# Kernel optimization log

Measured on AMD Instinct MI355X. Metric: run time of the kernel, lower is better.

## Reference

```python
import jax, jax.numpy as jnp
import numpy as np
from jax import lax

INPUT, HIDDEN, LAYERS, ACTIONS = 512, 128, 2, 10
B, T = 512, 256


def _lstm_layer(x_seq, Wih, Whh, bih, bhh):
    """x_seq: [B,T,D] -> (outputs [B,T,H], h_T [B,H], c_T [B,H]). PyTorch gate order i,f,g,o."""
    Bsz = x_seq.shape[0]
    H = Whh.shape[1]
    # Precompute input projection for all timesteps (one big GEMM).
    x_proj = jnp.einsum('btd,gd->btg', x_seq, Wih) + bih + bhh  # [B,T,4H]

    def step(carry, xt):
        h, c = carry
        gates = xt + h @ Whh.T  # [B,4H]
        i, f, g, o = jnp.split(gates, 4, axis=-1)
        c = jax.nn.sigmoid(f) * c + jax.nn.sigmoid(i) * jnp.tanh(g)
        h = jax.nn.sigmoid(o) * jnp.tanh(c)
        return (h, c), h

    init = (jnp.zeros((Bsz, H), x_seq.dtype), jnp.zeros((Bsz, H), x_seq.dtype))
    (hT, cT), hs = lax.scan(step, init, jnp.swapaxes(x_proj, 0, 1))  # hs: [T,B,H]
    return jnp.swapaxes(hs, 0, 1), hT, cT


def setup_inputs() -> dict:
    key = jax.random.key(0)
    ks = jax.random.split(key, 16)
    s_in = 1.0 / np.sqrt(HIDDEN)

    def u(k, shape):
        return jax.random.uniform(k, shape, jnp.float32, -s_in, s_in)

    return {
        'x': jax.random.normal(ks[0], (B, T, INPUT), jnp.float32),
        'Wih0': u(ks[1], (4 * HIDDEN, INPUT)),
        'Whh0': u(ks[2], (4 * HIDDEN, HIDDEN)),
        'bih0': u(ks[3], (4 * HIDDEN,)),
        'bhh0': u(ks[4], (4 * HIDDEN,)),
        'Wih1': u(ks[5], (4 * HIDDEN, HIDDEN)),
        'Whh1': u(ks[6], (4 * HIDDEN, HIDDEN)),
        'bih1': u(ks[7], (4 * HIDDEN,)),
        'bhh1': u(ks[8], (4 * HIDDEN,)),
        'fc1_w': u(ks[9], (HIDDEN // 2, HIDDEN)),
        'fc1_b': u(ks[10], (HIDDEN // 2,)),
        'fc2_w': u(ks[11], (ACTIONS, HIDDEN // 2)),
        'fc2_b': u(ks[12], (ACTIONS,)),
    }


def reference(x, Wih0, Whh0, bih0, bhh0, Wih1, Whh1, bih1, bhh1, fc1_w, fc1_b, fc2_w, fc2_b):
    # Layer 0 (input 512 -> hidden 128); dropout is inference-off (identity).
    h0_seq, h0, c0 = _lstm_layer(x, Wih0, Whh0, bih0, bhh0)
    # Layer 1 (hidden 128 -> hidden 128)
    h1_seq, h1, c1 = _lstm_layer(h0_seq, Wih1, Whh1, bih1, bhh1)
    last = h1_seq[:, -1, :]  # [B,H]
    hid = jax.nn.relu(last @ fc1_w.T + fc1_b)
    logits = hid @ fc2_w.T + fc2_b
    probs = jax.nn.softmax(logits, axis=-1)
    h_n = jnp.stack([h0, h1], axis=0)  # [num_layers,B,H]
    c_n = jnp.stack([c0, c1], axis=0)
    return probs, h_n, c_n
```

## Files before the change

kernel.cpp:

```cpp
#include <hip/hip_runtime.h>
#include <hip/hip_bf16.h>


#define BATCH 512
#define SEQT  256
#define INPUTD 512
#define HID   128
#define GATES 512
#define RB    4
#define SUBS  16
#define NCH   (SEQT / SUBS)

typedef __bf16 bf16_t;
typedef bf16_t bf16x4 __attribute__((ext_vector_type(4)));
typedef bf16_t bf16x8 __attribute__((ext_vector_type(8)));
typedef float  f32x4  __attribute__((ext_vector_type(4)));

__device__ __forceinline__ float sigm(float x) {
    return __builtin_amdgcn_rcpf(1.f + __expf(-x));
}
__device__ __forceinline__ float tanhfast(float x) {
    float xc = fminf(fmaxf(x, -15.f), 15.f);
    float e = __expf(2.f * xc);
    return (e - 1.f) * __builtin_amdgcn_rcpf(e + 1.f);
}

__global__ __launch_bounds__(256) void cvt_weights(
    const float* __restrict__ w0, const float* __restrict__ w1,
    const float* __restrict__ w2, const float* __restrict__ w3,
    bf16_t* __restrict__ o0, bf16_t* __restrict__ o1,
    bf16_t* __restrict__ o2, bf16_t* __restrict__ o3,
    unsigned* __restrict__ flags)
{
    int b = blockIdx.x;
    if (b == 448) {
        uint4 z = make_uint4(0u, 0u, 0u, 0u);
        #pragma unroll
        for (int i = 0; i < 4; ++i)
            ((uint4*)flags)[i * 256 + threadIdx.x] = z;
        return;
    }
    const float* src; bf16_t* dst; long base;
    if (b < 256)      { src = w0; dst = o0; base = (long)b * 256; }
    else if (b < 320) { src = w1; dst = o1; base = (long)(b - 256) * 256; }
    else if (b < 384) { src = w2; dst = o2; base = (long)(b - 320) * 256; }
    else              { src = w3; dst = o3; base = (long)(b - 384) * 256; }
    long i = base + threadIdx.x;
    float4 v = ((const float4*)src)[i];
    bf16x4 r;
    r[0] = (bf16_t)v.x; r[1] = (bf16_t)v.y;
    r[2] = (bf16_t)v.z; r[3] = (bf16_t)v.w;
    ((bf16x4*)dst)[i] = r;
}

__global__ __launch_bounds__(256) void gemm_mfma(
    const float* __restrict__ A, const bf16_t* __restrict__ W,
    const float* __restrict__ b1, const float* __restrict__ b2,
    float* __restrict__ out,
    int K, int tcs, int tcmask, int srcT, int t0)
{
    __shared__ bf16_t As[128 * 32];
    __shared__ bf16_t Bs[128 * 32];
    int tid = threadIdx.x;
    int l = tid & 63;
    int w = tid >> 6;
    int wm = w >> 1, wn = w & 1;
    int bn = blockIdx.x;
    int bm = blockIdx.y;
    int Tc = tcmask + 1;

    long aoff[2], boff[2];
    #pragma unroll
    for (int c = 0; c < 2; ++c) {
        int m = bm * 128 + (tid >> 2) + 64 * c;
        int xr = ((m >> tcs) * srcT) + t0 + (m & tcmask);
        aoff[c] = (long)xr * K + (tid & 3) * 8;
        int n = bn * 128 + (tid >> 2) + 64 * c;
        boff[c] = (long)n * K + (tid & 3) * 8;
    }

    f32x4 acc[4][4];
    #pragma unroll
    for (int i = 0; i < 4; ++i)
        #pragma unroll
        for (int j = 0; j < 4; ++j)
            acc[i][j] = (f32x4){0.f, 0.f, 0.f, 0.f};

    const int rbase = wm * 64 + (l & 15);
    const int cbase = wn * 64 + (l & 15);
    const int kfrag = (l >> 4) * 8;

    for (int kt = 0; kt < K; kt += 32) {
        float4 av[2][2];
        #pragma unroll
        for (int c = 0; c < 2; ++c) {
            av[c][0] = *(const float4*)(A + aoff[c] + kt);
            av[c][1] = *(const float4*)(A + aoff[c] + kt + 4);
        }
        __builtin_amdgcn_global_load_lds(
            (const __attribute__((address_space(1))) void*)(W + boff[0] + kt),
            (__attribute__((address_space(3))) void*)(Bs + tid * 8), 16, 0, 0);
        __builtin_amdgcn_global_load_lds(
            (const __attribute__((address_space(1))) void*)(W + boff[1] + kt),
            (__attribute__((address_space(3))) void*)(Bs + 2048 + tid * 8), 16, 0, 0);
        #pragma unroll
        for (int c = 0; c < 2; ++c) {
            bf16x8 ab;
            ab[0] = (bf16_t)av[c][0].x; ab[1] = (bf16_t)av[c][0].y;
            ab[2] = (bf16_t)av[c][0].z; ab[3] = (bf16_t)av[c][0].w;
            ab[4] = (bf16_t)av[c][1].x; ab[5] = (bf16_t)av[c][1].y;
            ab[6] = (bf16_t)av[c][1].z; ab[7] = (bf16_t)av[c][1].w;
            *(bf16x8*)(As + c * 2048 + tid * 8) = ab;
        }
        __syncthreads();

        bf16x8 af[4], bfr[4];
        #pragma unroll
        for (int i = 0; i < 4; ++i)
            af[i] = *(const bf16x8*)(As + (rbase + i * 16) * 32 + kfrag);
        #pragma unroll
        for (int j = 0; j < 4; ++j)
            bfr[j] = *(const bf16x8*)(Bs + (cbase + j * 16) * 32 + kfrag);

        #pragma unroll
        for (int i = 0; i < 4; ++i)
            #pragma unroll
            for (int j = 0; j < 4; ++j)
                acc[i][j] = __builtin_amdgcn_mfma_f32_16x16x32_bf16(
                    af[i], bfr[j], acc[i][j], 0, 0, 0);
        __syncthreads();
    }

    #pragma unroll
    for (int i = 0; i < 4; ++i) {
        int m0 = bm * 128 + wm * 64 + i * 16 + (l >> 4) * 4;
        #pragma unroll
        for (int j = 0; j < 4; ++j) {
            int n = bn * 128 + wn * 64 + j * 16 + (l & 15);
            float bb = b1[n] + b2[n];
            int hid = n & 127;
            #pragma unroll
            for (int r = 0; r < 4; ++r) {
                int m = m0 + r;
                int b = m >> tcs;
                int t = m & tcmask;
                int br = b >> 2, brow = b & 3;
                out[(((long)br * Tc + t) * 4 + bn) * 512 + brow * 128 + hid] =
                    acc[i][j][r] + bb;
            }
        }
    }
}

#define BARRIER_()                                                             \
    do {                                                                       \
        asm volatile("s_waitcnt lgkmcnt(0)" ::: "memory");                     \
        __builtin_amdgcn_s_barrier();                                          \
        __builtin_amdgcn_sched_barrier(0);                                     \
    } while (0)

#define REC0_STEP(X, t)                                                        \
    {                                                                          \
        bf16x8 a[4];                                                           \
        _Pragma("unroll")                                                      \
        for (int ks = 0; ks < 4; ++ks) {                                       \
            int ba = (col * 256 + ks * 64 + lgroup * 16) ^ ((col & 7) << 4);   \
            a[ks] = *(const bf16x8*)((const char*)h_lds + ba);                 \
        }                                                                      \
        f32x4 acc[4];                                                          \
        _Pragma("unroll")                                                      \
        for (int g = 0; g < 4; ++g) acc[g] = (f32x4){0.f, 0.f, 0.f, 0.f};      \
        _Pragma("unroll")                                                      \
        for (int ks = 0; ks < 4; ++ks)                                         \
            _Pragma("unroll")                                                  \
            for (int g = 0; g < 4; ++g)                                        \
                acc[g] = __builtin_amdgcn_mfma_f32_16x16x32_bf16(              \
                    a[ks], __builtin_bit_cast(bf16x8, wreg[g][ks]), acc[g],    \
                    0, 0, 0);                                                  \
        if (lgroup == 0) {                                                     \
            _Pragma("unroll")                                                  \
            for (int r = 0; r < 4; ++r) {                                      \
                f32x4 v;                                                       \
                v[0] = acc[0][r]; v[1] = acc[1][r];                            \
                v[2] = acc[2][r]; v[3] = acc[3][r];                            \
                *(f32x4*)((char*)g_lds + r * 2048 + coff * 16) = v;            \
            }                                                                  \
        }                                                                      \
        BARRIER_();                                                            \
        {                                                                      \
            f32x4 gv = *(const f32x4*)((const char*)g_lds + tid * 16);         \
            float zi = gv[0] + X.x, zf = gv[1] + X.y;                          \
            float zg = gv[2] + X.z, zo = gv[3] + X.w;                          \
            c = sigm(zf) * c + sigm(zi) * tanhfast(zg);                        \
            h = sigm(zo) * tanhfast(c);                                        \
            *(bf16_t*)((char*)h_lds + hba) = (bf16_t)h;                        \
            h0qp[(long)(t) * 512] = (bf16_t)h;                                 \
        }                                                                      \
        if ((t) + 2 < Tc) {                                                    \
            long o = (long)((t) + 2) * 2048;                                   \
            X.x = xpt[o];        X.y = xpt[o + 512];                           \
            X.z = xpt[o + 1024]; X.w = xpt[o + 1536];                          \
        }                                                                      \
        if (((t) & (SUBS - 1)) == SUBS - 1)                                    \
            asm volatile("s_waitcnt vmcnt(0)" ::: "memory");                   \
        BARRIER_();                                                            \
        if ((((t) & (SUBS - 1)) == SUBS - 1) && tid == 0) {                    \
            __threadfence();                                                   \
            __hip_atomic_store(flagp + ((t) >> 4), 1u, __ATOMIC_RELEASE,       \
                               __HIP_MEMORY_SCOPE_AGENT);                      \
        }                                                                      \
    }

__global__ __launch_bounds__(512, 2) void lstm_dual(
    const float* __restrict__ xp4,
    const bf16_t* __restrict__ Wh0,
    const bf16_t* __restrict__ Wi1,
    const bf16_t* __restrict__ Wh1,
    const float* __restrict__ bih1, const float* __restrict__ bhh1,
    bf16_t* __restrict__ h0q,
    unsigned* __restrict__ flags,
    float* __restrict__ h0st, float* __restrict__ c0st,
    float* __restrict__ h1st, float* __restrict__ c1st,
    int Tc, int first, int subbase)
{
    __shared__ __align__(16) char pool[28 * 1024];
    int tid = threadIdx.x;
    int l = tid & 63;
    int wv = tid >> 6;
    int pair = blockIdx.x & 127;
    int r0 = pair * RB;
    int col = l & 15;
    int lgroup = l >> 4;
    int kreg = lgroup * 8;
    int erow = tid >> 7, ehid = tid & 127;
    const int hba = (erow * 256 + ehid * 2) ^ ((erow & 7) << 4);
    unsigned* flagp = flags + pair * NCH + subbase;

    if (blockIdx.x < 128) {
        bf16_t* h_lds = (bf16_t*)pool;
        float*  g_lds = (float*)(pool + 4096);
        int coff = wv * 16 + col;

        f32x4 wreg[4][4];
        #pragma unroll
        for (int g = 0; g < 4; ++g)
            #pragma unroll
            for (int ks = 0; ks < 4; ++ks)
                wreg[g][ks] = *(const f32x4*)(Wh0 + (long)(g * 128 + coff) * HID
                                              + ks * 32 + kreg);
        #pragma unroll
        for (int g = 0; g < 4; ++g)
            #pragma unroll
            for (int ks = 0; ks < 4; ++ks)
                asm volatile("" : "+a"(wreg[g][ks]));

        float c = first ? 0.f : c0st[(r0 + erow) * HID + ehid];
        float h = first ? 0.f : h0st[(r0 + erow) * HID + ehid];

        ((float2*)h_lds)[tid & 255] = make_float2(0.f, 0.f);
        __syncthreads();
        *(bf16_t*)((char*)h_lds + hba) = (bf16_t)h;
        __syncthreads();

        const float* xpt = xp4 + (long)pair * Tc * 2048 + tid;
        bf16_t* h0qp = h0q + (long)pair * Tc * 512 + (hba >> 1);
        float4 xA, xB;
        xA.x = xpt[0];    xA.y = xpt[512];
        xA.z = xpt[1024]; xA.w = xpt[1536];
        if (Tc > 1) {
            xB.x = xpt[2048];        xB.y = xpt[2048 + 512];
            xB.z = xpt[2048 + 1024]; xB.w = xpt[2048 + 1536];
        } else {
            xB = make_float4(0.f, 0.f, 0.f, 0.f);
        }

        for (int tt = 0; tt < Tc; tt += 2) {
            REC0_STEP(xA, tt)
            REC0_STEP(xB, tt + 1)
        }

        h0st[(r0 + erow) * HID + ehid] = h;
        c0st[(r0 + erow) * HID + ehid] = c;
    } else {
        bf16_t* h0stg = (bf16_t*)pool;
        bf16_t* h1_lds = (bf16_t*)(pool + 8192);
        float*  g1a = (float*)(pool + 12288);
        float*  g1b = (float*)(pool + 20480);
        int isWi = wv < 4;
        int w4 = wv & 3;
        int coff1 = w4 * 32;

        const bf16_t* Wsrc = isWi ? Wi1 : Wh1;
        f32x4 wreg[2][4][4];
        #pragma unroll
        for (int c2 = 0; c2 < 2; ++c2)
            #pragma unroll
            for (int g = 0; g < 4; ++g)
                #pragma unroll
                for (int ks = 0; ks < 4; ++ks)
                    wreg[c2][g][ks] = *(const f32x4*)(
                        Wsrc + (long)(g * 128 + coff1 + c2 * 16 + col) * HID
                        + ks * 32 + kreg);
        #pragma unroll
        for (int c2 = 0; c2 < 2; ++c2)
            #pragma unroll
            for (int g = 0; g < 4; ++g)
                #pragma unroll
                for (int ks = 0; ks < 4; ++ks)
                    asm volatile("" : "+a"(wreg[c2][g][ks]));

        float4 bias1;
        bias1.x = bih1[ehid]       + bhh1[ehid];
        bias1.y = bih1[128 + ehid] + bhh1[128 + ehid];
        bias1.z = bih1[256 + ehid] + bhh1[256 + ehid];
        bias1.w = bih1[384 + ehid] + bhh1[384 + ehid];

        float c1 = first ? 0.f : c1st[(r0 + erow) * HID + ehid];
        float h1 = first ? 0.f : h1st[(r0 + erow) * HID + ehid];

        ((float2*)pool)[tid] = make_float2(0.f, 0.f);
        ((float2*)pool)[tid + 512] = make_float2(0.f, 0.f);
        ((float2*)(pool + 8192))[tid & 255] = make_float2(0.f, 0.f);
        __syncthreads();
        *(bf16_t*)((char*)h1_lds + hba) = (bf16_t)h1;
        __syncthreads();

        if (wv == 0) {
            while (__hip_atomic_load(flagp, __ATOMIC_ACQUIRE,
                                     __HIP_MEMORY_SCOPE_AGENT) == 0u)
                __builtin_amdgcn_s_sleep(2);
            __builtin_amdgcn_global_load_lds(
                (const __attribute__((address_space(1))) void*)(
                    h0q + (long)pair * Tc * 512 + l * 8),
                (__attribute__((address_space(3))) void*)h0stg, 16, 0, 0);
            asm volatile("s_waitcnt vmcnt(0)" ::: "memory");
        }
        __syncthreads();

        for (int t = 0; t < Tc; ++t) {
            int pw = (t + 1) & 3;
            if (t + 1 < Tc && wv == pw) {
                if (((t + 1) & (SUBS - 1)) == 0) {
                    unsigned* fp = flagp + ((t + 1) >> 4);
                    while (__hip_atomic_load(fp, __ATOMIC_ACQUIRE,
                                             __HIP_MEMORY_SCOPE_AGENT) == 0u)
                        __builtin_amdgcn_s_sleep(2);
                }
                __builtin_amdgcn_global_load_lds(
                    (const __attribute__((address_space(1))) void*)(
                        h0q + ((long)pair * Tc + t + 1) * 512 + l * 8),
                    (__attribute__((address_space(3))) void*)(
                        h0stg + ((t + 1) & 1) * 2048), 16, 0, 0);
            }

            const char* asrc = isWi
                ? (const char*)(h0stg + (t & 1) * 2048)
                : (const char*)h1_lds;
            bf16x8 a[4];
            #pragma unroll
            for (int ks = 0; ks < 4; ++ks) {
                int ba = (col * 256 + ks * 64 + lgroup * 16) ^ ((col & 7) << 4);
                a[ks] = *(const bf16x8*)(asrc + ba);
            }
            float* gdst = isWi ? g1a : g1b;
            #pragma unroll
            for (int c2 = 0; c2 < 2; ++c2) {
                f32x4 acc[4];
                #pragma unroll
                for (int g = 0; g < 4; ++g) acc[g] = (f32x4){0.f, 0.f, 0.f, 0.f};
                #pragma unroll
                for (int ks = 0; ks < 4; ++ks)
                    #pragma unroll
                    for (int g = 0; g < 4; ++g)
                        acc[g] = __builtin_amdgcn_mfma_f32_16x16x32_bf16(
                            a[ks], __builtin_bit_cast(bf16x8, wreg[c2][g][ks]),
                            acc[g], 0, 0, 0);
                if (lgroup == 0) {
                    #pragma unroll
                    for (int r = 0; r < 4; ++r) {
                        f32x4 v;
                        v[0] = acc[0][r]; v[1] = acc[1][r];
                        v[2] = acc[2][r]; v[3] = acc[3][r];
                        *(f32x4*)((char*)gdst + r * 2048 +
                                  (coff1 + c2 * 16 + col) * 16) = v;
                    }
                }
            }
            BARRIER_();

            {
                f32x4 gva = *(const f32x4*)((const char*)g1a + tid * 16);
                f32x4 gvb = *(const f32x4*)((const char*)g1b + tid * 16);
                float zi = gva[0] + gvb[0] + bias1.x;
                float zf = gva[1] + gvb[1] + bias1.y;
                float zg = gva[2] + gvb[2] + bias1.z;
                float zo = gva[3] + gvb[3] + bias1.w;
                c1 = sigm(zf) * c1 + sigm(zi) * tanhfast(zg);
                h1 = sigm(zo) * tanhfast(c1);
                *(bf16_t*)((char*)h1_lds + hba) = (bf16_t)h1;
            }
            if (t + 1 < Tc && wv == pw)
                asm volatile("s_waitcnt vmcnt(0)" ::: "memory");
            BARRIER_();
        }

        h1st[(r0 + erow) * HID + ehid] = h1;
        c1st[(r0 + erow) * HID + ehid] = c1;
    }
}

__global__ __launch_bounds__(128) void fc_head(
    const float* __restrict__ h0st, const float* __restrict__ c0st,
    const float* __restrict__ h1st, const float* __restrict__ c1st,
    const float* __restrict__ fc1w, const float* __restrict__ fc1b,
    const float* __restrict__ fc2w, const float* __restrict__ fc2b,
    float* __restrict__ out)
{
    __shared__ float h1_s[HID];
    __shared__ float hid_s[64];
    __shared__ float log_s[10];
    int t = threadIdx.x;
    int b = blockIdx.x;

    h1_s[t] = h1st[b * HID + t];
    __syncthreads();

    if (t < 64) {
        float a = fc1b[t];
        const float* wrow = fc1w + t * HID;
        #pragma unroll 4
        for (int k = 0; k < HID; ++k) a = fmaf(wrow[k], h1_s[k], a);
        hid_s[t] = fmaxf(a, 0.f);
    }
    __syncthreads();

    if (t < 10) {
        float a = fc2b[t];
        const float* wrow = fc2w + t * 64;
        #pragma unroll 4
        for (int k = 0; k < 64; ++k) a = fmaf(wrow[k], hid_s[k], a);
        log_s[t] = a;
    }
    __syncthreads();

    if (t == 0) {
        float m = log_s[0];
        #pragma unroll
        for (int j = 1; j < 10; ++j) m = fmaxf(m, log_s[j]);
        float e[10];
        float s = 0.f;
        #pragma unroll
        for (int j = 0; j < 10; ++j) { e[j] = __expf(log_s[j] - m); s += e[j]; }
        float inv = __builtin_amdgcn_rcpf(s);
        #pragma unroll
        for (int j = 0; j < 10; ++j) out[b * 10 + j] = e[j] * inv;
    }

    float* hn = out + BATCH * 10;
    float* cn = hn + 2 * BATCH * HID;
    hn[b * HID + t] = h0st[b * HID + t];
    hn[BATCH * HID + b * HID + t] = h1_s[t];
    cn[b * HID + t] = c0st[b * HID + t];
    cn[BATCH * HID + b * HID + t] = c1st[b * HID + t];
}

extern "C" void kernel_launch(void* const* d_in, const int* in_sizes, int n_in,
                              void* d_out, int out_size, void* d_ws, size_t ws_size,
                              hipStream_t stream) {
    const float* x    = (const float*)d_in[0];
    const float* Wih0 = (const float*)d_in[1];
    const float* Whh0 = (const float*)d_in[2];
    const float* bih0 = (const float*)d_in[3];
    const float* bhh0 = (const float*)d_in[4];
    const float* Wih1 = (const float*)d_in[5];
    const float* Whh1 = (const float*)d_in[6];
    const float* bih1 = (const float*)d_in[7];
    const float* bhh1 = (const float*)d_in[8];
    const float* fc1w = (const float*)d_in[9];
    const float* fc1b = (const float*)d_in[10];
    const float* fc2w = (const float*)d_in[11];
    const float* fc2b = (const float*)d_in[12];
    float* out = (float*)d_out;

    int Tc = SEQT;
    while (Tc > SUBS) {
        size_t need = (size_t)BATCH * Tc * GATES * 4
                    + ((size_t)GATES * INPUTD + 3 * (size_t)GATES * HID) * 2
                    + (size_t)128 * Tc * 512 * 2
                    + 4 * (size_t)BATCH * HID * 4
                    + 128 * NCH * 4 + 512;
        if (need <= ws_size) break;
        Tc >>= 1;
    }
    int tcs = __builtin_ctz((unsigned)Tc);

    float*    xp   = (float*)d_ws;
    bf16_t*   wb0  = (bf16_t*)(xp + (size_t)BATCH * Tc * GATES);
    bf16_t*   wb1  = wb0 + (size_t)GATES * INPUTD;
    bf16_t*   wh0b = wb1 + (size_t)GATES * HID;
    bf16_t*   wh1b = wh0b + (size_t)GATES * HID;
    bf16_t*   h0q  = wh1b + (size_t)GATES * HID;
    float*    h0st = (float*)(h0q + (size_t)128 * Tc * 512);
    float*    c0st = h0st + (size_t)BATCH * HID;
    float*    h1st = c0st + (size_t)BATCH * HID;
    float*    c1st = h1st + (size_t)BATCH * HID;
    unsigned* flags = (unsigned*)(c1st + (size_t)BATCH * HID);

    cvt_weights<<<449, 256, 0, stream>>>(Wih0, Wih1, Whh0, Whh1,
                                         wb0, wb1, wh0b, wh1b, flags);

    int nchunk = SEQT / Tc;
    dim3 gemm_grid(GATES / 128, (BATCH * Tc) / 128);

    for (int ci = 0; ci < nchunk; ++ci) {
        gemm_mfma<<<gemm_grid, 256, 0, stream>>>(
            x, wb0, bih0, bhh0, xp, INPUTD, tcs, Tc - 1, SEQT, ci * Tc);
        lstm_dual<<<256, 512, 0, stream>>>(
            xp, wh0b, wb1, wh1b, bih1, bhh1, h0q, flags,
            h0st, c0st, h1st, c1st, Tc, ci == 0, ci * (Tc / SUBS));
    }

    fc_head<<<BATCH, 128, 0, stream>>>(
        h0st, c0st, h1st, c1st, fc1w, fc1b, fc2w, fc2b, out);
}
```

Measured before the change: 586.7 us.

## Move layer-1 input projection into layer-0 recurrence block, stream fp32 gate preactivations

The layer-0 block now also holds the layer-1 input weights and computes Wi1·h0 alongside its own recurrent MFMA, writing fp32 gate preactivations for layer 1 to global memory. The layer-1 block then runs only its own recurrent MFMA and reads those preactivations behind chunk flags, instead of staging h0 through LDS and splitting waves between two GEMMs. This shortens the layer-1 critical path per step and frees LDS. In exchange, layer 0 does twice the MFMA work per step, needs more accumulator registers, and writes a 4x larger fp32 intermediate buffer, which may also shrink the time-chunk size when workspace is tight.

Result: slower. 850.1 us (+44.9%).

```diff
diff --git a/kernel.cpp b/kernel.cpp
--- a/kernel.cpp
+++ b/kernel.cpp
@@ -160,6 +160,72 @@
     } while (0)
 
 #define REC0_STEP(X, t)                                                        \
+    {                                                                          \
+        bf16x8 a[4];                                                           \
+        _Pragma("unroll")                                                      \
+        for (int ks = 0; ks < 4; ++ks) {                                       \
+            int ba = (col * 256 + ks * 64 + lgroup * 16) ^ ((col & 7) << 4);   \
+            a[ks] = *(const bf16x8*)((const char*)h_lds + ba);                 \
+        }                                                                      \
+        f32x4 acc0[4], acc1[4];                                                \
+        _Pragma("unroll")                                                      \
+        for (int g = 0; g < 4; ++g) {                                          \
+            acc0[g] = (f32x4){0.f, 0.f, 0.f, 0.f};                             \
+            acc1[g] = (f32x4){0.f, 0.f, 0.f, 0.f};                             \
+        }                                                                      \
+        _Pragma("unroll")                                                      \
+        for (int ks = 0; ks < 4; ++ks)                                         \
+            _Pragma("unroll")                                                  \
+            for (int g = 0; g < 4; ++g) {                                      \
+                acc0[g] = __builtin_amdgcn_mfma_f32_16x16x32_bf16(             \
+                    a[ks], __builtin_bit_cast(bf16x8, wreg[g][ks]), acc0[g],   \
+                    0, 0, 0);                                                  \
+                acc1[g] = __builtin_amdgcn_mfma_f32_16x16x32_bf16(             \
+                    a[ks], __builtin_bit_cast(bf16x8, wi[g][ks]), acc1[g],     \
+                    0, 0, 0);                                                  \
+            }                                                                  \
+        if (lgroup == 0) {                                                     \
+            _Pragma("unroll")                                                  \
+            for (int r = 0; r < 4; ++r) {                                      \
+                f32x4 v;                                                       \
+                v[0] = acc0[0][r]; v[1] = acc0[1][r];                          \
+                v[2] = acc0[2][r]; v[3] = acc0[3][r];                          \
+                *(f32x4*)((char*)g_lds + r * 2048 + coff * 16) = v;            \
+            }                                                                  \
+            if ((t) > 0) {                                                     \
+                float* yt = yqbase + (long)((t) - 1) * 2048;                   \
+                _Pragma("unroll")                                              \
+                for (int g = 0; g < 4; ++g)                                    \
+                    _Pragma("unroll")                                          \
+                    for (int r = 0; r < 4; ++r)                                \
+                        yt[g * 512 + r * 128 + coff] = acc1[g][r];             \
+            }                                                                  \
+        }                                                                      \
+        if ((((t) & (SUBS - 1)) == 0) && (t) > 0)                              \
+            asm volatile("s_waitcnt vmcnt(0)" ::: "memory");                   \
+        BARRIER_();                                                            \
+        if ((((t) & (SUBS - 1)) == 0) && (t) > 0 && tid == 0) {                \
+            __threadfence();                                                   \
+            __hip_atomic_store(flagp + ((t) >> 4) - 1, 1u, __ATOMIC_RELEASE,   \
+                               __HIP_MEMORY_SCOPE_AGENT);                      \
+        }                                                                      \
+        {                                                                      \
+            f32x4 gv = *(const f32x4*)((const char*)g_lds + tid * 16);         \
+            float zi = gv[0] + X.x, zf = gv[1] + X.y;                          \
+            float zg = gv[2] + X.z, zo = gv[3] + X.w;                          \
+            c = sigm(zf) * c + sigm(zi) * tanhfast(zg);                        \
+            h = sigm(zo) * tanhfast(c);                                        \
+            *(bf16_t*)((char*)h_lds + hba) = (bf16_t)h;                        \
+        }                                                                      \
+        if ((t) + 2 < Tc) {                                                    \
+            long o = (long)((t) + 2) * 2048;                                   \
+            X.x = xpt[o];        X.y = xpt[o + 512];                           \
+            X.z = xpt[o + 1024]; X.w = xpt[o + 1536];                          \
+        }                                                                      \
+        BARRIER_();                                                            \
+    }
+
+#define REC1_STEP(Y, t)                                                        \
     {                                                                          \
         bf16x8 a[4];                                                           \
         _Pragma("unroll")                                                      \
@@ -189,26 +255,24 @@
         BARRIER_();                                                            \
         {                                                                      \
             f32x4 gv = *(const f32x4*)((const char*)g_lds + tid * 16);         \
-            float zi = gv[0] + X.x, zf = gv[1] + X.y;                          \
-            float zg = gv[2] + X.z, zo = gv[3] + X.w;                          \
+            float zi = gv[0] + Y.x + bias1.x, zf = gv[1] + Y.y + bias1.y;      \
+            float zg = gv[2] + Y.z + bias1.z, zo = gv[3] + Y.w + bias1.w;      \
             c = sigm(zf) * c + sigm(zi) * tanhfast(zg);                        \
             h = sigm(zo) * tanhfast(c);                                        \
             *(bf16_t*)((char*)h_lds + hba) = (bf16_t)h;                        \
-            h0qp[(long)(t) * 512] = (bf16_t)h;                                 \
         }                                                                      \
         if ((t) + 2 < Tc) {                                                    \
+            if ((((t) + 2) & (SUBS - 1)) == 0) {                               \
+                unsigned* fp = flagp + (((t) + 2) >> 4);                       \
+                while (__hip_atomic_load(fp, __ATOMIC_ACQUIRE,                 \
+                                         __HIP_MEMORY_SCOPE_AGENT) == 0u)      \
+                    __builtin_amdgcn_s_sleep(2);                               \
+            }                                                                  \
             long o = (long)((t) + 2) * 2048;                                   \
-            X.x = xpt[o];        X.y = xpt[o + 512];                           \
-            X.z = xpt[o + 1024]; X.w = xpt[o + 1536];                          \
-        }                                                                      \
-        if (((t) & (SUBS - 1)) == SUBS - 1)                                    \
-            asm volatile("s_waitcnt vmcnt(0)" ::: "memory");                   \
+            Y.x = yqt[o];        Y.y = yqt[o + 512];                           \
+            Y.z = yqt[o + 1024]; Y.w = yqt[o + 1536];                          \
+        }                                                                      \
         BARRIER_();                                                            \
-        if ((((t) & (SUBS - 1)) == SUBS - 1) && tid == 0) {                    \
-            __threadfence();                                                   \
-            __hip_atomic_store(flagp + ((t) >> 4), 1u, __ATOMIC_RELEASE,       \
-                               __HIP_MEMORY_SCOPE_AGENT);                      \
-        }                                                                      \
     }
 
 __global__ __launch_bounds__(512, 2) void lstm_dual(
@@ -217,13 +281,13 @@
     const bf16_t* __restrict__ Wi1,
     const bf16_t* __restrict__ Wh1,
     const float* __restrict__ bih1, const float* __restrict__ bhh1,
-    bf16_t* __restrict__ h0q,
+    float* __restrict__ yq,
     unsigned* __restrict__ flags,
     float* __restrict__ h0st, float* __restrict__ c0st,
     float* __restrict__ h1st, float* __restrict__ c1st,
     int Tc, int first, int subbase)
 {
-    __shared__ __align__(16) char pool[28 * 1024];
+    __shared__ __align__(16) char pool[12 * 1024];
     int tid = threadIdx.x;
     int l = tid & 63;
     int wv = tid >> 6;
@@ -232,27 +296,31 @@
     int col = l & 15;
     int lgroup = l >> 4;
     int kreg = lgroup * 8;
+    int coff = wv * 16 + col;
     int erow = tid >> 7, ehid = tid & 127;
     const int hba = (erow * 256 + ehid * 2) ^ ((erow & 7) << 4);
     unsigned* flagp = flags + pair * NCH + subbase;
 
+    bf16_t* h_lds = (bf16_t*)pool;
+    float*  g_lds = (float*)(pool + 4096);
+
     if (blockIdx.x < 128) {
-        bf16_t* h_lds = (bf16_t*)pool;
-        float*  g_lds = (float*)(pool + 4096);
-        int coff = wv * 16 + col;
-
-        f32x4 wreg[4][4];
+        f32x4 wreg[4][4], wi[4][4];
         #pragma unroll
         for (int g = 0; g < 4; ++g)
             #pragma unroll
-            for (int ks = 0; ks < 4; ++ks)
-                wreg[g][ks] = *(const f32x4*)(Wh0 + (long)(g * 128 + coff) * HID
-                                              + ks * 32 + kreg);
+            for (int ks = 0; ks < 4; ++ks) {
+                long o = (long)(g * 128 + coff) * HID + ks * 32 + kreg;
+                wreg[g][ks] = *(const f32x4*)(Wh0 + o);
+                wi[g][ks]   = *(const f32x4*)(Wi1 + o);
+            }
         #pragma unroll
         for (int g = 0; g < 4; ++g)
             #pragma unroll
-            for (int ks = 0; ks < 4; ++ks)
+            for (int ks = 0; ks < 4; ++ks) {
                 asm volatile("" : "+a"(wreg[g][ks]));
+                asm volatile("" : "+a"(wi[g][ks]));
+            }
 
         float c = first ? 0.f : c0st[(r0 + erow) * HID + ehid];
         float h = first ? 0.f : h0st[(r0 + erow) * HID + ehid];
@@ -263,7 +331,7 @@
         __syncthreads();
 
         const float* xpt = xp4 + (long)pair * Tc * 2048 + tid;
-        bf16_t* h0qp = h0q + (long)pair * Tc * 512 + (hba >> 1);
+        float* yqbase = yq + (long)pair * Tc * 2048;
         float4 xA, xB;
         xA.x = xpt[0];    xA.y = xpt[512];
         xA.z = xpt[1024]; xA.w = xpt[1536];
@@ -279,35 +347,55 @@
             REC0_STEP(xB, tt + 1)
         }
 
+        {
+            bf16x8 a[4];
+            #pragma unroll
+            for (int ks = 0; ks < 4; ++ks) {
+                int ba = (col * 256 + ks * 64 + lgroup * 16) ^ ((col & 7) << 4);
+                a[ks] = *(const bf16x8*)((const char*)h_lds + ba);
+            }
+            f32x4 acc1[4];
+            #pragma unroll
+            for (int g = 0; g < 4; ++g) acc1[g] = (f32x4){0.f, 0.f, 0.f, 0.f};
+            #pragma unroll
+            for (int ks = 0; ks < 4; ++ks)
+                #pragma unroll
+                for (int g = 0; g < 4; ++g)
+                    acc1[g] = __builtin_amdgcn_mfma_f32_16x16x32_bf16(
+                        a[ks], __builtin_bit_cast(bf16x8, wi[g][ks]), acc1[g],
+                        0, 0, 0);
+            if (lgroup == 0) {
+                float* yt = yqbase + (long)(Tc - 1) * 2048;
+                #pragma unroll
+                for (int g = 0; g < 4; ++g)
+                    #pragma unroll
+                    for (int r = 0; r < 4; ++r)
+                        yt[g * 512 + r * 128 + coff] = acc1[g][r];
+            }
+            asm volatile("s_waitcnt vmcnt(0)" ::: "memory");
+            BARRIER_();
+            if (tid == 0) {
+                __threadfence();
+                __hip_atomic_store(flagp + NCH - 1, 1u, __ATOMIC_RELEASE,
+                                   __HIP_MEMORY_SCOPE_AGENT);
+            }
+        }
+
         h0st[(r0 + erow) * HID + ehid] = h;
         c0st[(r0 + erow) * HID + ehid] = c;
     } else {
-        bf16_t* h0stg = (bf16_t*)pool;
-        bf16_t* h1_lds = (bf16_t*)(pool + 8192);
-        float*  g1a = (float*)(pool + 12288);
-        float*  g1b = (float*)(pool + 20480);
-        int isWi = wv < 4;
-        int w4 = wv & 3;
-        int coff1 = w4 * 32;
-
-        const bf16_t* Wsrc = isWi ? Wi1 : Wh1;
-        f32x4 wreg[2][4][4];
-        #pragma unroll
-        for (int c2 = 0; c2 < 2; ++c2)
-            #pragma unroll
-            for (int g = 0; g < 4; ++g)
-                #pragma unroll
-                for (int ks = 0; ks < 4; ++ks)
-                    wreg[c2][g][ks] = *(const f32x4*)(
-                        Wsrc + (long)(g * 128 + coff1 + c2 * 16 + col) * HID
-                        + ks * 32 + kreg);
-        #pragma unroll
-        for (int c2 = 0; c2 < 2; ++c2)
-            #pragma unroll
-            for (int g = 0; g < 4; ++g)
-                #pragma unroll
-                for (int ks = 0; ks < 4; ++ks)
-                    asm volatile("" : "+a"(wreg[c2][g][ks]));
+        f32x4 wreg[4][4];
+        #pragma unroll
+        for (int g = 0; g < 4; ++g)
+            #pragma unroll
+            for (int ks = 0; ks < 4; ++ks)
+                wreg[g][ks] = *(const f32x4*)(
+                    Wh1 + (long)(g * 128 + coff) * HID + ks * 32 + kreg);
+        #pragma unroll
+        for (int g = 0; g < 4; ++g)
+            #pragma unroll
+            for (int ks = 0; ks < 4; ++ks)
+                asm volatile("" : "+a"(wreg[g][ks]));
 
         float4 bias1;
         bias1.x = bih1[ehid]       + bhh1[ehid];
@@ -315,97 +403,35 @@
         bias1.z = bih1[256 + ehid] + bhh1[256 + ehid];
         bias1.w = bih1[384 + ehid] + bhh1[384 + ehid];
 
-        float c1 = first ? 0.f : c1st[(r0 + erow) * HID + ehid];
-        float h1 = first ? 0.f : h1st[(r0 + erow) * HID + ehid];
-
-        ((float2*)pool)[tid] = make_float2(0.f, 0.f);
-        ((float2*)pool)[tid + 512] = make_float2(0.f, 0.f);
-        ((float2*)(pool + 8192))[tid & 255] = make_float2(0.f, 0.f);
+        float c = first ? 0.f : c1st[(r0 + erow) * HID + ehid];
+        float h = first ? 0.f : h1st[(r0 + erow) * HID + ehid];
+
+        ((float2*)h_lds)[tid & 255] = make_float2(0.f, 0.f);
         __syncthreads();
-        *(bf16_t*)((char*)h1_lds + hba) = (bf16_t)h1;
+        *(bf16_t*)((char*)h_lds + hba) = (bf16_t)h;
         __syncthreads();
 
-        if (wv == 0) {
-            while (__hip_atomic_load(flagp, __ATOMIC_ACQUIRE,
-                                     __HIP_MEMORY_SCOPE_AGENT) == 0u)
-                __builtin_amdgcn_s_sleep(2);
-            __builtin_amdgcn_global_load_lds(
-                (const __attribute__((address_space(1))) void*)(
-                    h0q + (long)pair * Tc * 512 + l * 8),
-                (__attribute__((address_space(3))) void*)h0stg, 16, 0, 0);
-            asm volatile("s_waitcnt vmcnt(0)" ::: "memory");
-        }
-        __syncthreads();
-
-        for (int t = 0; t < Tc; ++t) {
-            int pw = (t + 1) & 3;
-            if (t + 1 < Tc && wv == pw) {
-                if (((t + 1) & (SUBS - 1)) == 0) {
-                    unsigned* fp = flagp + ((t + 1) >> 4);
-                    while (__hip_atomic_load(fp, __ATOMIC_ACQUIRE,
-                                             __HIP_MEMORY_SCOPE_AGENT) == 0u)
-                        __builtin_amdgcn_s_sleep(2);
-                }
-                __builtin_amdgcn_global_load_lds(
-                    (const __attribute__((address_space(1))) void*)(
-                        h0q + ((long)pair * Tc + t + 1) * 512 + l * 8),
-                    (__attribute__((address_space(3))) void*)(
-                        h0stg + ((t + 1) & 1) * 2048), 16, 0, 0);
-            }
-
-            const char* asrc = isWi
-                ? (const char*)(h0stg + (t & 1) * 2048)
-                : (const char*)h1_lds;
-            bf16x8 a[4];
-            #pragma unroll
-            for (int ks = 0; ks < 4; ++ks) {
-                int ba = (col * 256 + ks * 64 + lgroup * 16) ^ ((col & 7) << 4);
-                a[ks] = *(const bf16x8*)(asrc + ba);
-            }
-            float* gdst = isWi ? g1a : g1b;
-            #pragma unroll
-            for (int c2 = 0; c2 < 2; ++c2) {
-                f32x4 acc[4];
-                #pragma unroll
-                for (int g = 0; g < 4; ++g) acc[g] = (f32x4){0.f, 0.f, 0.f, 0.f};
-                #pragma unroll
-                for (int ks = 0; ks < 4; ++ks)
-                    #pragma unroll
-                    for (int g = 0; g < 4; ++g)
-                        acc[g] = __builtin_amdgcn_mfma_f32_16x16x32_bf16(
-                            a[ks], __builtin_bit_cast(bf16x8, wreg[c2][g][ks]),
-                            acc[g], 0, 0, 0);
-                if (lgroup == 0) {
-                    #pragma unroll
-                    for (int r = 0; r < 4; ++r) {
-                        f32x4 v;
-                        v[0] = acc[0][r]; v[1] = acc[1][r];
-                        v[2] = acc[2][r]; v[3] = acc[3][r];
-                        *(f32x4*)((char*)gdst + r * 2048 +
-                                  (coff1 + c2 * 16 + col) * 16) = v;
-                    }
-                }
-            }
-            BARRIER_();
-
-            {
-                f32x4 gva = *(const f32x4*)((const char*)g1a + tid * 16);
-                f32x4 gvb = *(const f32x4*)((const char*)g1b + tid * 16);
-                float zi = gva[0] + gvb[0] + bias1.x;
-                float zf = gva[1] + gvb[1] + bias1.y;
-                float zg = gva[2] + gvb[2] + bias1.z;
-                float zo = gva[3] + gvb[3] + bias1.w;
-                c1 = sigm(zf) * c1 + sigm(zi) * tanhfast(zg);
-                h1 = sigm(zo) * tanhfast(c1);
-                *(bf16_t*)((char*)h1_lds + hba) = (bf16_t)h1;
-            }
-            if (t + 1 < Tc && wv == pw)
-                asm volatile("s_waitcnt vmcnt(0)" ::: "memory");
-            BARRIER_();
-        }
-
-        h1st[(r0 + erow) * HID + ehid] = h1;
-        c1st[(r0 + erow) * HID + ehid] = c1;
+        const float* yqt = yq + (long)pair * Tc * 2048 + tid;
+        while (__hip_atomic_load(flagp, __ATOMIC_ACQUIRE,
+                                 __HIP_MEMORY_SCOPE_AGENT) == 0u)
+            __builtin_amdgcn_s_sleep(2);
+        float4 yA, yB;
+        yA.x = yqt[0];    yA.y = yqt[512];
+        yA.z = yqt[1024]; yA.w = yqt[1536];
+        if (Tc > 1) {
+            yB.x = yqt[2048];        yB.y = yqt[2048 + 512];
+            yB.z = yqt[2048 + 1024]; yB.w = yqt[2048 + 1536];
+        } else {
+            yB = make_float4(0.f, 0.f, 0.f, 0.f);
+        }
+
+        for (int tt = 0; tt < Tc; tt += 2) {
+            REC1_STEP(yA, tt)
+            REC1_STEP(yB, tt + 1)
+        }
+
+        h1st[(r0 + erow) * HID + ehid] = h;
+        c1st[(r0 + erow) * HID + ehid] = c;
     }
 }
 
@@ -486,9 +512,9 @@
     while (Tc > SUBS) {
         size_t need = (size_t)BATCH * Tc * GATES * 4
                     + ((size_t)GATES * INPUTD + 3 * (size_t)GATES * HID) * 2
-                    + (size_t)128 * Tc * 512 * 2
+                    + (size_t)128 * Tc * 2048 * 4
                     + 4 * (size_t)BATCH * HID * 4
-                    + 128 * NCH * 4 + 512;
+                    + 128 * 2 * NCH * 4 + 512;
         if (need <= ws_size) break;
         Tc >>= 1;
     }
@@ -499,8 +525,8 @@
     bf16_t*   wb1  = wb0 + (size_t)GATES * INPUTD;
     bf16_t*   wh0b = wb1 + (size_t)GATES * HID;
     bf16_t*   wh1b = wh0b + (size_t)GATES * HID;
-    bf16_t*   h0q  = wh1b + (size_t)GATES * HID;
-    float*    h0st = (float*)(h0q + (size_t)128 * Tc * 512);
+    float*    yq   = (float*)(wh1b + (size_t)GATES * HID);
+    float*    h0st = yq + (size_t)128 * Tc * 2048;
     float*    c0st = h0st + (size_t)BATCH * HID;
     float*    h1st = c0st + (size_t)BATCH * HID;
     float*    c1st = h1st + (size_t)BATCH * HID;
@@ -516,7 +542,7 @@
         gemm_mfma<<<gemm_grid, 256, 0, stream>>>(
             x, wb0, bih0, bhh0, xp, INPUTD, tcs, Tc - 1, SEQT, ci * Tc);
         lstm_dual<<<256, 512, 0, stream>>>(
-            xp, wh0b, wb1, wh1b, bih1, bhh1, h0q, flags,
+            xp, wh0b, wb1, wh1b, bih1, bhh1, yq, flags,
             h0st, c0st, h1st, c1st, Tc, ci == 0, ci * (Tc / SUBS));
     }
 
```
